# Optimization experiments

Measured on AMD Instinct MI355X. Metric: run time of the kernel, lower is better.

The kernel has to match this reference:

```python
import jax, jax.numpy as jnp
import numpy as np

B = 16
D_MODEL = 1024
HALF = D_MODEL // 2
PATTERN_NUM = 4096
PATTERN_LEN = 32          # == patch_seq_len
ENC_SEQ = 2048
SIM_NUM = 64
NUM_PATCH = ENC_SEQ // PATTERN_LEN


def setup_inputs() -> dict:
    key = jax.random.key(0)
    ks = jax.random.split(key, 6)
    w = lambda k, shape: jax.random.normal(k, shape, jnp.float32) * 0.02
    return {
        "src": jax.random.normal(ks[0], (B, ENC_SEQ, D_MODEL), jnp.float32),
        "meta_pattern_pool": jax.random.normal(ks[1], (PATTERN_NUM, PATTERN_LEN), jnp.float32),
        "fuse_w": w(ks[2], (PATTERN_LEN * HALF, SIM_NUM)),
        "fuse_b": jnp.zeros((SIM_NUM,), jnp.float32),
        "recover_w": w(ks[3], (SIM_NUM, HALF)),
        "recover_b": jnp.zeros((HALF,), jnp.float32),
        "gp_w": w(ks[4], (HALF, 10)),
        "gp_b": jnp.zeros((10,), jnp.float32),
    }


def reference(src, meta_pattern_pool, fuse_w, fuse_b, recover_w, recover_b, gp_w, gp_b):
    # src: [B, S, D]; take second half of channels and split into patches
    x = src[:, :, HALF:].reshape(B, NUM_PATCH, PATTERN_LEN, HALF)  # [B,P,L,H]

    # per-patch similarity score against pattern pool (vectorized over patches)
    low = jnp.mean(x @ gp_w + gp_b, axis=-1)                       # [B,P,L]
    scores = jnp.einsum('bpl,nl->bpn', low, meta_pattern_pool)     # [B,P,N]

    # topk pattern retrieval; original uses batch-0 indices for all batches
    _, idx = jax.lax.top_k(scores, SIM_NUM)                        # [B,P,S]
    selected = meta_pattern_pool[idx[0]]                           # [P,S,L]

    # softmax routing key per patch
    logits = x.reshape(B, NUM_PATCH, PATTERN_LEN * HALF) @ fuse_w + fuse_b
    route = jax.nn.softmax(logits, axis=-1)                        # [B,P,S]

    # fuse[b,p,l,s] = route[b,p,s] * selected[p,s,l]
    fuse = route[:, :, None, :] * jnp.transpose(selected, (0, 2, 1))[None]  # [B,P,L,S]
    out = (fuse @ recover_w + recover_b).reshape(B, ENC_SEQ, HALF)

    padding = jnp.einsum('bps,psl->bpl', route, selected).reshape(B, ENC_SEQ)

    out_full = jnp.concatenate([src[:, :, :HALF], out], axis=-1)   # [B,S,D]
    # original prepends an uninitialized torch.empty buffer; we use zeros
    padding_out = jnp.concatenate([jnp.zeros((B, ENC_SEQ), src.dtype), padding], axis=-1)
    return out_full, padding_out
```

## Files before the change

kernel.cpp:

```cpp
#include <hip/hip_runtime.h>
#include <hip/hip_bf16.h>

#define NB 16
#define DMODEL 1024
#define HALFD 512
#define PNUM 4096
#define PLEN 32
#define SEQ 2048
#define SIM 64
#define NPATCH 64
#define NROWS (NB*SEQ)
#define MROWS (NB*NPATCH)
#define KDIM (PLEN*HALFD)
#define NCOPY 512
#define OUT0 ((size_t)NB*SEQ*DMODEL)

typedef __attribute__((ext_vector_type(8))) short s8v;
typedef __attribute__((ext_vector_type(4))) float f32x4;
typedef __attribute__((ext_vector_type(8))) unsigned short ush8;
typedef unsigned long long u64;

__device__ __forceinline__ unsigned short f2bf(float f) {
    __hip_bfloat16 h = __float2bfloat16(f);
    return *reinterpret_cast<unsigned short*>(&h);
}
__device__ __forceinline__ u64 umax64(u64 a, u64 b) { return a > b ? a : b; }
__device__ __forceinline__ u64 umin64(u64 a, u64 b) { return a < b ? a : b; }
__device__ __forceinline__ u64 clean6(u64 v, int lane) {
    #pragma unroll
    for (int j = 32; j; j >>= 1) {
        u64 o = __shfl_xor(v, j);
        v = ((lane & j) == 0) ? umax64(v, o) : umin64(v, o);
    }
    return v;
}

union PrepShared {
    struct { double gpm[513]; double lowp[PLEN]; u64 wl[4][64]; } tk;
    float tile[64][68];
};
__global__ __launch_bounds__(256) void k_prep(
        const float* __restrict__ gp_w, const float* __restrict__ gp_b,
        const float* __restrict__ fw, const float* __restrict__ rw,
        const float* __restrict__ src, const float* __restrict__ pool,
        unsigned short* __restrict__ fwT, unsigned short* __restrict__ rwf,
        u64* __restrict__ cand) {
    __shared__ PrepShared u;
    int bid = blockIdx.x, t = threadIdx.x;
    int lane = t & 63, w = t >> 6;
    if (bid < 512) {
        int p = bid >> 3, q = bid & 7;
        for (int h = t; h < HALFD; h += 256) {
            double s = 0.0;
            #pragma unroll
            for (int j = 0; j < 10; ++j) s += (double)gp_w[h*10 + j];
            u.tk.gpm[h] = s / 10.0;
        }
        if (t == 0) {
            double sb = 0.0;
            #pragma unroll
            for (int j = 0; j < 10; ++j) sb += (double)gp_b[j];
            u.tk.gpm[512] = sb / 10.0;
        }
        __syncthreads();
        {
            const double* g0 = u.tk.gpm + lane*4;
            const double* g1 = u.tk.gpm + 256 + lane*4;
            #pragma unroll
            for (int rr = 0; rr < 8; ++rr) {
                int r = w*8 + rr;
                const float4* s4 = reinterpret_cast<const float4*>(src + (size_t)(p*PLEN + r)*DMODEL);
                float4 x0 = s4[128 + lane], x1 = s4[192 + lane];
                double d = (double)x0.x*g0[0] + (double)x0.y*g0[1] + (double)x0.z*g0[2] + (double)x0.w*g0[3]
                         + (double)x1.x*g1[0] + (double)x1.y*g1[1] + (double)x1.z*g1[2] + (double)x1.w*g1[3];
                #pragma unroll
                for (int o = 32; o; o >>= 1) d += __shfl_xor(d, o);
                if (lane == 0) u.tk.lowp[r] = d + u.tk.gpm[512];
            }
        }
        __syncthreads();
        u64 v[2];
        #pragma unroll
        for (int cc = 0; cc < 2; ++cc) {
            int n = q*512 + (w*2 + cc)*64 + lane;
            const float4* p4 = reinterpret_cast<const float4*>(pool + (size_t)n*PLEN);
            double s = 0.0;
            #pragma unroll
            for (int r2 = 0; r2 < 8; ++r2) {
                float4 vv = p4[r2];
                s += (double)vv.x*u.tk.lowp[r2*4] + (double)vv.y*u.tk.lowp[r2*4+1]
                   + (double)vv.z*u.tk.lowp[r2*4+2] + (double)vv.w*u.tk.lowp[r2*4+3];
            }
            u64 ub = (u64)__double_as_longlong(s);
            u64 okey = ub ^ (((u64)((long long)ub >> 63)) | 0x8000000000000000ULL);
            v[cc] = (okey & ~0xFFFULL) | (u64)(0xFFF - n);
        }
        #pragma unroll
        for (int kk = 2; kk <= 64; kk <<= 1) {
            #pragma unroll
            for (int j = kk >> 1; j; j >>= 1) {
                #pragma unroll
                for (int cc = 0; cc < 2; ++cc) {
                    u64 o = __shfl_xor(v[cc], j);
                    bool keepMax = ((lane & kk) == 0) == ((lane & j) == 0);
                    v[cc] = keepMax ? umax64(v[cc], o) : umin64(v[cc], o);
                }
            }
        }
        u64 rb2 = __shfl(v[1], 63 - lane);
        u64 m = umax64(v[0], rb2);
        m = clean6(m, lane);
        u.tk.wl[w][lane] = m;
        __syncthreads();
        if (w == 0) {
            u64 a = umax64(u.tk.wl[0][lane], u.tk.wl[1][63 - lane]); a = clean6(a, lane);
            u64 b = umax64(u.tk.wl[2][lane], u.tk.wl[3][63 - lane]); b = clean6(b, lane);
            u64 r2 = __shfl(b, 63 - lane);
            u64 f = umax64(a, r2); f = clean6(f, lane);
            cand[(size_t)(p*8 + q)*SIM + lane] = f;
        }
    } else if (bid < 768) {
        int k0 = (bid - 512) * 64;
        int i = t >> 2;
        #pragma unroll
        for (int q = 0; q < 4; ++q) {
            int c = (t & 3) + q*4;
            float4 v = *reinterpret_cast<const float4*>(fw + (size_t)(k0 + i)*SIM + c*4);
            *reinterpret_cast<float4*>(&u.tile[i][c*4]) = v;
        }
        __syncthreads();
        #pragma unroll
        for (int c2 = 0; c2 < 2; ++c2) {
            int e = c2*256 + t;
            int kl = e >> 8, fn = (e >> 6) & 3, l = e & 63;
            int kk0 = kl*32 + ((l >> 4) * 8), n = fn*16 + (l & 15);
            ush8 hv;
            #pragma unroll
            for (int j = 0; j < 8; ++j) hv[j] = f2bf(u.tile[kk0 + j][n]);
            size_t dst = ((size_t)((2*(bid - 512) + kl)*4 + fn)*64 + l)*8;
            *reinterpret_cast<ush8*>(fwT + dst) = hv;
        }
    } else {
        int q = t >> 6;
        int idx = (bid - 768)*4 + q;
        int ks = idx >> 5, fn = idx & 31;
        int ml = lane & 15, kg = lane >> 4;
        ush8 hv;
        #pragma unroll
        for (int j = 0; j < 8; ++j)
            hv[j] = f2bf(rw[(size_t)(ks*32 + kg*8 + j)*HALFD + fn*16 + ml]);
        size_t dst = ((size_t)idx*64 + lane)*8;
        *reinterpret_cast<ush8*>(rwf + dst) = hv;
    }
}

__global__ __launch_bounds__(256) void k_logits(
        const float* __restrict__ src, const unsigned short* __restrict__ fwT,
        const u64* __restrict__ cand, float* __restrict__ part,
        int* __restrict__ sel, int nks) {
    int t = threadIdx.x, lane = t & 63, w = t >> 6;
    int bid = blockIdx.x;
    int NL = 16*nks;
    if (bid >= NL) {
        if (w != 0) return;
        int p = bid - NL;
        const u64* c = cand + (size_t)p*8*SIM;
        u64 a = umax64(c[lane],         c[1*SIM + 63 - lane]); a = clean6(a, lane);
        u64 bq = umax64(c[2*SIM + lane], c[3*SIM + 63 - lane]); bq = clean6(bq, lane);
        u64 d = umax64(c[4*SIM + lane], c[5*SIM + 63 - lane]); d = clean6(d, lane);
        u64 e = umax64(c[6*SIM + lane], c[7*SIM + 63 - lane]); e = clean6(e, lane);
        u64 ab = umax64(a, __shfl(bq, 63 - lane)); ab = clean6(ab, lane);
        u64 de = umax64(d, __shfl(e, 63 - lane)); de = clean6(de, lane);
        u64 f  = umax64(ab, __shfl(de, 63 - lane)); f = clean6(f, lane);
        sel[p*SIM + lane] = 0xFFF - (int)(f & 0xFFFULL);
        return;
    }
    int mt = bid / nks, ks = bid - mt*nks;
    int kchunk = KDIM / nks, nstep = kchunk >> 6;
    int r0 = mt*64;
    int ml = lane & 15, kg = lane >> 4;
    int Rrow = r0 + w*16 + ml;
    int bb = Rrow >> 6, prow = Rrow & 63;
    const float* xrow = src + ((size_t)(bb*SEQ + prow*PLEN))*DMODEL + HALFD;
    int kblk_base = (ks*kchunk) >> 5;
    f32x4 acc[4] = {};
    for (int step = 0; step < nstep; ++step) {
        int k0 = ks*kchunk + step*64;
        int l = k0 >> 9, h0 = k0 & 511;
        const float* ap = xrow + (size_t)l*DMODEL + h0 + kg*8;
        float4 va0 = *reinterpret_cast<const float4*>(ap);
        float4 va1 = *reinterpret_cast<const float4*>(ap + 4);
        float4 vb0 = *reinterpret_cast<const float4*>(ap + 32);
        float4 vb1 = *reinterpret_cast<const float4*>(ap + 36);
        s8v ah0, ah1;
        float fa[8] = {va0.x,va0.y,va0.z,va0.w,va1.x,va1.y,va1.z,va1.w};
        float fbv[8] = {vb0.x,vb0.y,vb0.z,vb0.w,vb1.x,vb1.y,vb1.z,vb1.w};
        #pragma unroll
        for (int j = 0; j < 8; ++j) {
            ah0[j] = (short)f2bf(fa[j]);
            ah1[j] = (short)f2bf(fbv[j]);
        }
        int kblk0 = kblk_base + step*2;
        #pragma unroll
        for (int fn = 0; fn < 4; ++fn) {
            size_t off0 = ((size_t)(kblk0*4 + fn)*64 + lane)*8;
            size_t off1 = ((size_t)((kblk0+1)*4 + fn)*64 + lane)*8;
            s8v bh0 = *reinterpret_cast<const s8v*>(fwT + off0);
            s8v bh1 = *reinterpret_cast<const s8v*>(fwT + off1);
            acc[fn] = __builtin_amdgcn_mfma_f32_16x16x32_bf16(ah0, bh0, acc[fn], 0, 0, 0);
            acc[fn] = __builtin_amdgcn_mfma_f32_16x16x32_bf16(ah1, bh1, acc[fn], 0, 0, 0);
        }
    }
    float* pout = part + (size_t)(mt*nks + ks)*4096;
    #pragma unroll
    for (int fn = 0; fn < 4; ++fn)
        #pragma unroll
        for (int r = 0; r < 4; ++r)
            pout[(w*16 + kg*4 + r)*64 + fn*16 + ml] = acc[fn][r];
}

union OutShared {
    struct { float A_T[SIM][36]; float routeS[64]; int selS[64]; float psum[4][64]; } a;
    float xpose[16][516];
};
__global__ __launch_bounds__(256) void k_out(
        const float* __restrict__ part, const float* __restrict__ fb,
        const int* __restrict__ sel, const float* __restrict__ pool,
        const unsigned short* __restrict__ rwf, const float* __restrict__ rb,
        const float* __restrict__ src, float* __restrict__ out,
        float* __restrict__ pad, int nks) {
    __shared__ OutShared u;
    int t = threadIdx.x, lane = t & 63, w = t >> 6;
    if (blockIdx.x < NCOPY) {
        int cb = blockIdx.x;
        size_t total = (size_t)NROWS * 128;
        const float4* s4 = reinterpret_cast<const float4*>(src);
        float4* o4 = reinterpret_cast<float4*>(out);
        for (size_t idx = (size_t)cb*256 + t; idx < total; idx += (size_t)NCOPY*256) {
            size_t r = idx >> 7, c = idx & 127;
            o4[r*256 + c] = s4[r*256 + c];
        }
        return;
    }
    int row = blockIdx.x - NCOPY;
    int b = row >> 6, p = row & 63;
    int kpw = nks >> 2;
    {
        float v = 0.f;
        for (int kq = 0; kq < kpw; ++kq) {
            int ks = w*kpw + kq;
            v += part[(size_t)(b*nks + ks)*4096 + p*64 + lane];
        }
        u.a.psum[w][lane] = v;
    }
    __syncthreads();
    if (w == 0) {
        float v = u.a.psum[0][lane] + u.a.psum[1][lane] + u.a.psum[2][lane] + u.a.psum[3][lane] + fb[lane];
        float m = v;
        #pragma unroll
        for (int o = 32; o; o >>= 1) m = fmaxf(m, __shfl_xor(m, o));
        float e = expf(v - m);
        float sum = e;
        #pragma unroll
        for (int o = 32; o; o >>= 1) sum += __shfl_xor(sum, o);
        u.a.routeS[lane] = e / sum;
    } else if (w == 1) {
        u.a.selS[lane] = sel[p*SIM + lane];
    }
    __syncthreads();
    #pragma unroll
    for (int q = 0; q < 8; ++q) {
        int e = t + q*256;
        int s = e >> 5, l = e & 31;
        u.a.A_T[s][l] = u.a.routeS[s] * pool[(size_t)u.a.selS[s]*PLEN + l];
    }
    __syncthreads();
    if (t < 32) {
        float ps = 0.f;
        #pragma unroll
        for (int s = 0; s < 64; ++s) ps += u.a.A_T[s][t];
        pad[(size_t)b*2*SEQ + SEQ + p*PLEN + t] = ps;
    } else if (t < 64) {
        pad[(size_t)b*2*SEQ + p*PLEN + (t - 32)] = 0.f;
    }
    int ml = lane & 15, kg = lane >> 4;
    s8v ah[2][2];
    #pragma unroll
    for (int mt = 0; mt < 2; ++mt)
        #pragma unroll
        for (int ks = 0; ks < 2; ++ks) {
            #pragma unroll
            for (int j = 0; j < 8; ++j)
                ah[mt][ks][j] = (short)f2bf(u.a.A_T[ks*32 + kg*8 + j][mt*16 + ml]);
        }
    f32x4 accA[8], accB[8];
    #pragma unroll
    for (int nt = 0; nt < 8; ++nt) {
        int fng = w*8 + nt;
        f32x4 acc0 = {}, acc1 = {};
        #pragma unroll
        for (int ks = 0; ks < 2; ++ks) {
            size_t off = ((size_t)(ks*32 + fng)*64 + lane)*8;
            s8v bh = *reinterpret_cast<const s8v*>(rwf + off);
            acc0 = __builtin_amdgcn_mfma_f32_16x16x32_bf16(ah[0][ks], bh, acc0, 0, 0, 0);
            acc1 = __builtin_amdgcn_mfma_f32_16x16x32_bf16(ah[1][ks], bh, acc1, 0, 0, 0);
        }
        float bias = rb[fng*16 + ml];
        #pragma unroll
        for (int r = 0; r < 4; ++r) { acc0[r] += bias; acc1[r] += bias; }
        accA[nt] = acc0; accB[nt] = acc1;
    }
    size_t orow0 = ((size_t)(b*SEQ + p*PLEN))*DMODEL + HALFD;
    #pragma unroll
    for (int mt = 0; mt < 2; ++mt) {
        __syncthreads();
        #pragma unroll
        for (int nt = 0; nt < 8; ++nt) {
            f32x4 a = (mt == 0) ? accA[nt] : accB[nt];
            #pragma unroll
            for (int r = 0; r < 4; ++r)
                u.xpose[kg*4 + r][w*128 + nt*16 + ml] = a[r];
        }
        __syncthreads();
        #pragma unroll
        for (int q = 0; q < 8; ++q) {
            int e = q*256 + t;
            int rr = e >> 7, c4 = e & 127;
            float4 v = *reinterpret_cast<float4*>(&u.xpose[rr][c4*4]);
            *reinterpret_cast<float4*>(out + orow0 + (size_t)(mt*16 + rr)*DMODEL + c4*4) = v;
        }
    }
}

static const void* by_size(void* const* d_in, const int* in_sizes, int n_in,
                           int want, int fallback) {
    for (int i = 0; i < n_in; ++i) if (in_sizes[i] == want) return d_in[i];
    return d_in[fallback];
}

extern "C" void kernel_launch(void* const* d_in, const int* in_sizes, int n_in,
                              void* d_out, int out_size, void* d_ws, size_t ws_size,
                              hipStream_t stream) {
    const float* src  = (const float*)by_size(d_in, in_sizes, n_in, NB*SEQ*DMODEL, 0);
    const float* pool = (const float*)by_size(d_in, in_sizes, n_in, PNUM*PLEN, 1);
    const float* fw   = (const float*)by_size(d_in, in_sizes, n_in, KDIM*SIM, 2);
    const float* fb   = (const float*)by_size(d_in, in_sizes, n_in, SIM, 3);
    const float* rw   = (const float*)by_size(d_in, in_sizes, n_in, SIM*HALFD, 4);
    const float* rb   = (const float*)by_size(d_in, in_sizes, n_in, HALFD, 5);
    const float* gpw  = (const float*)by_size(d_in, in_sizes, n_in, HALFD*10, 6);
    const float* gpb  = (const float*)by_size(d_in, in_sizes, n_in, 10, 7);
    float* out = (float*)d_out;
    float* pad = out + OUT0;

    int nks = (ws_size >= (size_t)(16u << 20)) ? 32 : 8;

    unsigned short* fwT = (unsigned short*)d_ws;
    unsigned short* rwf = fwT + (size_t)SIM*KDIM;
    u64*   cand  = (u64*)(rwf + (size_t)SIM*HALFD);
    int*   sel   = (int*)(cand + (size_t)NPATCH*8*SIM);
    float* part  = (float*)(sel + 4096);

    hipLaunchKernelGGL(k_prep,   dim3(784),    dim3(256), 0, stream,
                       gpw, gpb, fw, rw, src, pool, fwT, rwf, cand);
    hipLaunchKernelGGL(k_logits, dim3(16*nks + NPATCH), dim3(256), 0, stream,
                       src, fwT, cand, part, sel, nks);
    hipLaunchKernelGGL(k_out,    dim3(NCOPY + MROWS), dim3(256), 0, stream,
                       part, fb, sel, pool, rwf, rb, src, out, pad, nks);
}
```

Baseline: 88.95 us.

## Split weight packing from top-k scoring and fuse candidate merge into output kernel

Weight packing (fuse_w and recover_w to bf16 fragments) now runs in its own small kernel. The per-patch pattern scoring and partial top-k move into the logits kernel as extra blocks, so they run alongside the split-K GEMM. The final 8-way candidate merge, which was a separate block group in the logits kernel, is now done inside the output kernel. This shortens the critical path of the first kernel and removes the sel buffer. The cost is that every output row (1024 blocks) repeats the merge for its patch instead of doing it once per patch.

```diff
diff --git a/kernel.cpp b/kernel.cpp
--- a/kernel.cpp
+++ b/kernel.cpp
@@ -35,37 +35,75 @@
     return v;
 }
 
-union PrepShared {
-    struct { double gpm[513]; double lowp[PLEN]; u64 wl[4][64]; } tk;
-    float tile[64][68];
-};
-__global__ __launch_bounds__(256) void k_prep(
+__global__ __launch_bounds__(256) void k_pack(
+        const float* __restrict__ fw, const float* __restrict__ rw,
+        unsigned short* __restrict__ fwT, unsigned short* __restrict__ rwf) {
+    __shared__ float tile[64][68];
+    int bid = blockIdx.x, t = threadIdx.x;
+    int lane = t & 63;
+    if (bid < 256) {
+        int k0 = bid * 64;
+        int i = t >> 2;
+        #pragma unroll
+        for (int q = 0; q < 4; ++q) {
+            int c = (t & 3) + q*4;
+            float4 v = *reinterpret_cast<const float4*>(fw + (size_t)(k0 + i)*SIM + c*4);
+            *reinterpret_cast<float4*>(&tile[i][c*4]) = v;
+        }
+        __syncthreads();
+        #pragma unroll
+        for (int c2 = 0; c2 < 2; ++c2) {
+            int e = c2*256 + t;
+            int kl = e >> 8, fn = (e >> 6) & 3, l = e & 63;
+            int kk0 = kl*32 + ((l >> 4) * 8), n = fn*16 + (l & 15);
+            ush8 hv;
+            #pragma unroll
+            for (int j = 0; j < 8; ++j) hv[j] = f2bf(tile[kk0 + j][n]);
+            size_t dst = ((size_t)((2*bid + kl)*4 + fn)*64 + l)*8;
+            *reinterpret_cast<ush8*>(fwT + dst) = hv;
+        }
+    } else {
+        int q = t >> 6;
+        int idx = (bid - 256)*4 + q;
+        int ks = idx >> 5, fn = idx & 31;
+        int ml = lane & 15, kg = lane >> 4;
+        ush8 hv;
+        #pragma unroll
+        for (int j = 0; j < 8; ++j)
+            hv[j] = f2bf(rw[(size_t)(ks*32 + kg*8 + j)*HALFD + fn*16 + ml]);
+        size_t dst = ((size_t)idx*64 + lane)*8;
+        *reinterpret_cast<ush8*>(rwf + dst) = hv;
+    }
+}
+
+__global__ __launch_bounds__(256) void k_mid(
+        const float* __restrict__ src, const unsigned short* __restrict__ fwT,
+        const float* __restrict__ pool,
         const float* __restrict__ gp_w, const float* __restrict__ gp_b,
-        const float* __restrict__ fw, const float* __restrict__ rw,
-        const float* __restrict__ src, const float* __restrict__ pool,
-        unsigned short* __restrict__ fwT, unsigned short* __restrict__ rwf,
-        u64* __restrict__ cand) {
-    __shared__ PrepShared u;
-    int bid = blockIdx.x, t = threadIdx.x;
-    int lane = t & 63, w = t >> 6;
-    if (bid < 512) {
-        int p = bid >> 3, q = bid & 7;
+        float* __restrict__ part, u64* __restrict__ cand, int nks) {
+    int t = threadIdx.x, lane = t & 63, w = t >> 6;
+    int bid = blockIdx.x;
+    int NL = 16*nks;
+    if (bid >= NL) {
+        __shared__ struct { double gpm[513]; double lowp[PLEN]; u64 wl[4][64]; } u;
+        int tb = bid - NL;
+        int p = tb >> 3, q = tb & 7;
         for (int h = t; h < HALFD; h += 256) {
             double s = 0.0;
             #pragma unroll
             for (int j = 0; j < 10; ++j) s += (double)gp_w[h*10 + j];
-            u.tk.gpm[h] = s / 10.0;
+            u.gpm[h] = s / 10.0;
         }
         if (t == 0) {
             double sb = 0.0;
             #pragma unroll
             for (int j = 0; j < 10; ++j) sb += (double)gp_b[j];
-            u.tk.gpm[512] = sb / 10.0;
+            u.gpm[512] = sb / 10.0;
         }
         __syncthreads();
         {
-            const double* g0 = u.tk.gpm + lane*4;
-            const double* g1 = u.tk.gpm + 256 + lane*4;
+            const double* g0 = u.gpm + lane*4;
+            const double* g1 = u.gpm + 256 + lane*4;
             #pragma unroll
             for (int rr = 0; rr < 8; ++rr) {
                 int r = w*8 + rr;
@@ -75,7 +113,7 @@
                          + (double)x1.x*g1[0] + (double)x1.y*g1[1] + (double)x1.z*g1[2] + (double)x1.w*g1[3];
                 #pragma unroll
                 for (int o = 32; o; o >>= 1) d += __shfl_xor(d, o);
-                if (lane == 0) u.tk.lowp[r] = d + u.tk.gpm[512];
+                if (lane == 0) u.lowp[r] = d + u.gpm[512];
             }
         }
         __syncthreads();
@@ -88,8 +126,8 @@
             #pragma unroll
             for (int r2 = 0; r2 < 8; ++r2) {
                 float4 vv = p4[r2];
-                s += (double)vv.x*u.tk.lowp[r2*4] + (double)vv.y*u.tk.lowp[r2*4+1]
-                   + (double)vv.z*u.tk.lowp[r2*4+2] + (double)vv.w*u.tk.lowp[r2*4+3];
+                s += (double)vv.x*u.lowp[r2*4] + (double)vv.y*u.lowp[r2*4+1]
+                   + (double)vv.z*u.lowp[r2*4+2] + (double)vv.w*u.lowp[r2*4+3];
             }
             u64 ub = (u64)__double_as_longlong(s);
             u64 okey = ub ^ (((u64)((long long)ub >> 63)) | 0x8000000000000000ULL);
@@ -110,69 +148,15 @@
         u64 rb2 = __shfl(v[1], 63 - lane);
         u64 m = umax64(v[0], rb2);
         m = clean6(m, lane);
-        u.tk.wl[w][lane] = m;
+        u.wl[w][lane] = m;
         __syncthreads();
         if (w == 0) {
-            u64 a = umax64(u.tk.wl[0][lane], u.tk.wl[1][63 - lane]); a = clean6(a, lane);
-            u64 b = umax64(u.tk.wl[2][lane], u.tk.wl[3][63 - lane]); b = clean6(b, lane);
+            u64 a = umax64(u.wl[0][lane], u.wl[1][63 - lane]); a = clean6(a, lane);
+            u64 b = umax64(u.wl[2][lane], u.wl[3][63 - lane]); b = clean6(b, lane);
             u64 r2 = __shfl(b, 63 - lane);
             u64 f = umax64(a, r2); f = clean6(f, lane);
             cand[(size_t)(p*8 + q)*SIM + lane] = f;
         }
-    } else if (bid < 768) {
-        int k0 = (bid - 512) * 64;
-        int i = t >> 2;
-        #pragma unroll
-        for (int q = 0; q < 4; ++q) {
-            int c = (t & 3) + q*4;
-            float4 v = *reinterpret_cast<const float4*>(fw + (size_t)(k0 + i)*SIM + c*4);
-            *reinterpret_cast<float4*>(&u.tile[i][c*4]) = v;
-        }
-        __syncthreads();
-        #pragma unroll
-        for (int c2 = 0; c2 < 2; ++c2) {
-            int e = c2*256 + t;
-            int kl = e >> 8, fn = (e >> 6) & 3, l = e & 63;
-            int kk0 = kl*32 + ((l >> 4) * 8), n = fn*16 + (l & 15);
-            ush8 hv;
-            #pragma unroll
-            for (int j = 0; j < 8; ++j) hv[j] = f2bf(u.tile[kk0 + j][n]);
-            size_t dst = ((size_t)((2*(bid - 512) + kl)*4 + fn)*64 + l)*8;
-            *reinterpret_cast<ush8*>(fwT + dst) = hv;
-        }
-    } else {
-        int q = t >> 6;
-        int idx = (bid - 768)*4 + q;
-        int ks = idx >> 5, fn = idx & 31;
-        int ml = lane & 15, kg = lane >> 4;
-        ush8 hv;
-        #pragma unroll
-        for (int j = 0; j < 8; ++j)
-            hv[j] = f2bf(rw[(size_t)(ks*32 + kg*8 + j)*HALFD + fn*16 + ml]);
-        size_t dst = ((size_t)idx*64 + lane)*8;
-        *reinterpret_cast<ush8*>(rwf + dst) = hv;
-    }
-}
-
-__global__ __launch_bounds__(256) void k_logits(
-        const float* __restrict__ src, const unsigned short* __restrict__ fwT,
-        const u64* __restrict__ cand, float* __restrict__ part,
-        int* __restrict__ sel, int nks) {
-    int t = threadIdx.x, lane = t & 63, w = t >> 6;
-    int bid = blockIdx.x;
-    int NL = 16*nks;
-    if (bid >= NL) {
-        if (w != 0) return;
-        int p = bid - NL;
-        const u64* c = cand + (size_t)p*8*SIM;
-        u64 a = umax64(c[lane],         c[1*SIM + 63 - lane]); a = clean6(a, lane);
-        u64 bq = umax64(c[2*SIM + lane], c[3*SIM + 63 - lane]); bq = clean6(bq, lane);
-        u64 d = umax64(c[4*SIM + lane], c[5*SIM + 63 - lane]); d = clean6(d, lane);
-        u64 e = umax64(c[6*SIM + lane], c[7*SIM + 63 - lane]); e = clean6(e, lane);
-        u64 ab = umax64(a, __shfl(bq, 63 - lane)); ab = clean6(ab, lane);
-        u64 de = umax64(d, __shfl(e, 63 - lane)); de = clean6(de, lane);
-        u64 f  = umax64(ab, __shfl(de, 63 - lane)); f = clean6(f, lane);
-        sel[p*SIM + lane] = 0xFFF - (int)(f & 0xFFFULL);
         return;
     }
     int mt = bid / nks, ks = bid - mt*nks;
@@ -225,7 +209,7 @@
 };
 __global__ __launch_bounds__(256) void k_out(
         const float* __restrict__ part, const float* __restrict__ fb,
-        const int* __restrict__ sel, const float* __restrict__ pool,
+        const u64* __restrict__ cand, const float* __restrict__ pool,
         const unsigned short* __restrict__ rwf, const float* __restrict__ rb,
         const float* __restrict__ src, float* __restrict__ out,
         float* __restrict__ pad, int nks) {
@@ -265,7 +249,15 @@
         for (int o = 32; o; o >>= 1) sum += __shfl_xor(sum, o);
         u.a.routeS[lane] = e / sum;
     } else if (w == 1) {
-        u.a.selS[lane] = sel[p*SIM + lane];
+        const u64* c = cand + (size_t)p*8*SIM;
+        u64 a = umax64(c[lane],         c[1*SIM + 63 - lane]); a = clean6(a, lane);
+        u64 bq = umax64(c[2*SIM + lane], c[3*SIM + 63 - lane]); bq = clean6(bq, lane);
+        u64 d = umax64(c[4*SIM + lane], c[5*SIM + 63 - lane]); d = clean6(d, lane);
+        u64 e = umax64(c[6*SIM + lane], c[7*SIM + 63 - lane]); e = clean6(e, lane);
+        u64 ab = umax64(a, __shfl(bq, 63 - lane)); ab = clean6(ab, lane);
+        u64 de = umax64(d, __shfl(e, 63 - lane)); de = clean6(de, lane);
+        u64 f  = umax64(ab, __shfl(de, 63 - lane)); f = clean6(f, lane);
+        u.a.selS[lane] = 0xFFF - (int)(f & 0xFFFULL);
     }
     __syncthreads();
     #pragma unroll
@@ -357,13 +349,11 @@
     unsigned short* fwT = (unsigned short*)d_ws;
     unsigned short* rwf = fwT + (size_t)SIM*KDIM;
     u64*   cand  = (u64*)(rwf + (size_t)SIM*HALFD);
-    int*   sel   = (int*)(cand + (size_t)NPATCH*8*SIM);
-    float* part  = (float*)(sel + 4096);
-
-    hipLaunchKernelGGL(k_prep,   dim3(784),    dim3(256), 0, stream,
-                       gpw, gpb, fw, rw, src, pool, fwT, rwf, cand);
-    hipLaunchKernelGGL(k_logits, dim3(16*nks + NPATCH), dim3(256), 0, stream,
-                       src, fwT, cand, part, sel, nks);
-    hipLaunchKernelGGL(k_out,    dim3(NCOPY + MROWS), dim3(256), 0, stream,
-                       part, fb, sel, pool, rwf, rb, src, out, pad, nks);
-}
+    float* part  = (float*)(cand + (size_t)NPATCH*8*SIM);
+
+    hipLaunchKernelGGL(k_pack, dim3(272),          dim3(256), 0, stream, fw, rw, fwT, rwf);
+    hipLaunchKernelGGL(k_mid,  dim3(16*nks + 512), dim3(256), 0, stream,
+                       src, fwT, pool, gpw, gpb, part, cand, nks);
+    hipLaunchKernelGGL(k_out,  dim3(NCOPY + MROWS), dim3(256), 0, stream,
+                       part, fb, cand, pool, rwf, rb, src, out, pad, nks);
+}
```

Result: faster. 84.42 us, median of 2 (-5.1%).
